# Kernel tuning notes

Measured on AMD Instinct MI355X. Metric: run time of the kernel, lower is better.

Reference implementation:

```python
import jax, jax.numpy as jnp
import numpy as np


def _conv2d(x, w, stride, padding):
    # x: NCHW, w: OIHW
    return jax.lax.conv_general_dilated(
        x, w, window_strides=(stride, stride),
        padding=((padding, padding), (padding, padding)),
        dimension_numbers=('NCHW', 'OIHW', 'NCHW'))


def setup_inputs() -> dict:
    key = jax.random.key(0)
    k1, k2 = jax.random.split(key)
    B, C_in, H, Wd = 8, 64, 256, 256
    C_out, ksz = 64, 3
    x = jax.random.normal(k1, (B, C_in, H, Wd), dtype=jnp.float32)
    W = jax.random.normal(k2, (C_out, C_in, ksz, ksz), dtype=jnp.float32)
    b = jnp.zeros((C_out,), dtype=jnp.float32)
    return {"x": x, "W": W, "b": b}


def reference(x, W, b):
    stride, padding = 1, 1
    B, C, H, Wd = x.shape
    # per-pixel (across-channel) normalization of activations
    xf = jnp.transpose(x, (0, 2, 3, 1)).reshape(-1, C)       # [B*H*W, C]
    mu = jnp.mean(xf, axis=-1, keepdims=True)
    var = jnp.mean((xf - mu) ** 2, axis=-1, keepdims=True)    # unbiased=False
    r = 1.0 / jnp.sqrt(var + 1e-8)
    y_norm = r * (xf - mu)
    # int8 fake-quant per pixel
    s_act = 127.0 / jnp.maximum(jnp.max(jnp.abs(y_norm), axis=-1, keepdims=True), 1e-8)
    y_tilde = jnp.clip(jnp.round(s_act * y_norm), -128.0, 127.0) / s_act
    y4 = jnp.transpose(y_tilde.reshape(B, H, Wd, C), (0, 3, 1, 2))
    # ternary weight quant (value; STE only matters for backward)
    s_w = 1.0 / jnp.maximum(jnp.mean(jnp.abs(W)), 1e-8)
    w_tilde = jnp.clip(jnp.round(s_w * W), -1.0, 1.0) / s_w
    out = _conv2d(y4, w_tilde, stride, padding) + b[None, :, None, None]
    return out
```

## Files before the change

kernel.cpp:

```cpp
#include <hip/hip_runtime.h>
#include <hip/hip_bf16.h>

typedef _Float16 half8 __attribute__((ext_vector_type(8)));
typedef float    f32x4 __attribute__((ext_vector_type(4)));

#define NB   8
#define NC   64
#define NH   256
#define NW   256
#define NO   64
#define Y_OFF    0ull
#define Y_BYTES  (33554432ull * 2ull)
#define TW_OFF   (Y_OFF + Y_BYTES)
#define TW_BYTES (576ull * 64ull * 2ull)
#define MSW_OFF  (TW_OFF + TW_BYTES)

__global__ __launch_bounds__(256) void wq_kernel(const float* __restrict__ W,
                                                 _Float16* __restrict__ tw2,
                                                 float* __restrict__ msw_out) {
    __shared__ float red[256];
    __shared__ float sw_sh;
    int tid = threadIdx.x;
    float s = 0.0f;
    #pragma unroll
    for (int i = 0; i < 144; ++i) s += fabsf(W[i * 256 + tid]);
    red[tid] = s;
    __syncthreads();
    for (int off = 128; off > 0; off >>= 1) {
        if (tid < off) red[tid] += red[tid + off];
        __syncthreads();
    }
    if (tid == 0) {
        float mean = red[0] / 36864.0f;
        float msw  = fmaxf(mean, 1e-8f);
        sw_sh      = 1.0f / msw;
        msw_out[0] = msw;
    }
    __syncthreads();
    float s_w = sw_sh;
    #pragma unroll
    for (int i = 0; i < 144; ++i) {
        int idx = i * 256 + tid;
        float t = rintf(s_w * W[idx]);
        t = fminf(1.0f, fmaxf(-1.0f, t));
        int o  = idx / 576;
        int r  = idx - o * 576;
        int c  = r / 9;
        int r2 = r - c * 9;
        int kh = r2 / 3;
        int kw = r2 - kh * 3;
        int k  = (kh * 3 + kw) * 64 + c;
        tw2[((k >> 3) * 64 + o) * 8 + (k & 7)] = (_Float16)t;
    }
}

__global__ __launch_bounds__(256, 2) void norm_kernel(const float* __restrict__ x,
                                                      _Float16* __restrict__ y) {
    int p  = blockIdx.x * 256 + threadIdx.x;
    int bb = p >> 16;
    int hw = p & 65535;
    const float* xp = x + (size_t)bb * 64 * 65536 + hw;

    float v[64];
    float s = 0.0f;
    #pragma unroll
    for (int c = 0; c < 64; ++c) { v[c] = xp[(size_t)c * 65536]; s += v[c]; }
    float mu = s * (1.0f / 64.0f);

    float var = 0.0f, dmax = 0.0f;
    #pragma unroll
    for (int c = 0; c < 64; ++c) {
        float d = v[c] - mu;
        var += d * d;
        dmax = fmaxf(dmax, fabsf(d));
    }
    var *= (1.0f / 64.0f);
    float r    = 1.0f / sqrtf(var + 1e-8f);
    float amax = fmaxf(dmax * r, 1e-8f);
    float s_a  = 127.0f / amax;
    float invs = amax / 127.0f;

    half8 hv[8];
    #pragma unroll
    for (int c = 0; c < 64; ++c) {
        float yn = (v[c] - mu) * r;
        float q  = rintf(s_a * yn);
        q = fminf(127.0f, fmaxf(-128.0f, q));
        hv[c >> 3][c & 7] = (_Float16)(q * invs);
    }
    half8* yp = (half8*)(y + (size_t)p * 64);
    #pragma unroll
    for (int j = 0; j < 8; ++j) yp[j] = hv[j];
}

__global__ __launch_bounds__(256, 2) void conv_kernel(const _Float16* __restrict__ y,
                                                      const _Float16* __restrict__ tw2,
                                                      const float* __restrict__ msw_p,
                                                      const float* __restrict__ bias,
                                                      float* __restrict__ out) {
    __shared__ alignas(16) _Float16 lds[3 * 8 * 66 * 8];

    int tid = threadIdx.x;
    int bid = blockIdx.x;
    int wt = bid & 3;
    int h  = (bid >> 2) & 255;
    int bb = bid >> 10;
    int w0 = wt * 64;

    for (int i = tid; i < 1584; i += 256) {
        int cc = i & 7;
        int t8 = i >> 3;
        int wl = t8 % 66;
        int kh = t8 / 66;
        int hp = h + kh - 1;
        int wp = w0 + wl - 1;
        half8 val;
        #pragma unroll
        for (int e = 0; e < 8; ++e) val[e] = (_Float16)0.0f;
        if ((unsigned)hp < 256u && (unsigned)wp < 256u)
            val = *(const half8*)(y + ((((size_t)bb * 256 + hp) * 256 + wp) * 64 + cc * 8));
        *(half8*)(lds + ((kh * 8 + cc) * 66 + wl) * 8) = val;
    }

    int l   = tid & 63;
    int wv  = tid >> 6;
    int l15 = l & 15;
    int q8  = l >> 4;

    half8 aw[18];
    #pragma unroll
    for (int ks = 0; ks < 18; ++ks)
        aw[ks] = *(const half8*)(tw2 + (((ks * 4 + q8) * 64) + wv * 16 + l15) * 8);

    __syncthreads();

    f32x4 acc[4];
    #pragma unroll
    for (int nt = 0; nt < 4; ++nt)
        #pragma unroll
        for (int r2 = 0; r2 < 4; ++r2) acc[nt][r2] = 0.0f;

    #pragma unroll
    for (int ks = 0; ks < 18; ++ks) {
        int tap = ks >> 1;
        int kh  = tap / 3;
        int kw  = tap - kh * 3;
        int ccb = (ks & 1) * 4 + q8;
        int base = ((kh * 8 + ccb) * 66 + kw + l15) * 8;
        #pragma unroll
        for (int nt = 0; nt < 4; ++nt) {
            half8 bf = *(const half8*)(lds + base + nt * 128);
            acc[nt] = __builtin_amdgcn_mfma_f32_16x16x32_f16(aw[ks], bf, acc[nt], 0, 0, 0);
        }
    }

    float msw = *msw_p;
    size_t obase = ((size_t)bb * 64) * 65536 + (size_t)h * 256;
    #pragma unroll
    for (int reg = 0; reg < 4; ++reg) {
        int o = wv * 16 + q8 * 4 + reg;
        float bo = bias[o];
        #pragma unroll
        for (int nt = 0; nt < 4; ++nt) {
            int w = w0 + nt * 16 + l15;
            out[obase + (size_t)o * 65536 + w] = acc[nt][reg] * msw + bo;
        }
    }
}

extern "C" void kernel_launch(void* const* d_in, const int* in_sizes, int n_in,
                              void* d_out, int out_size, void* d_ws, size_t ws_size,
                              hipStream_t stream) {
    const float* x = (const float*)d_in[0];
    const float* W = (const float*)d_in[1];
    const float* b = (const float*)d_in[2];
    float* out = (float*)d_out;

    char* ws = (char*)d_ws;
    _Float16* y   = (_Float16*)(ws + Y_OFF);
    _Float16* tw2 = (_Float16*)(ws + TW_OFF);
    float*    msw = (float*)(ws + MSW_OFF);

    wq_kernel<<<1, 256, 0, stream>>>(W, tw2, msw);
    norm_kernel<<<2048, 256, 0, stream>>>(x, y);
    conv_kernel<<<8192, 256, 0, stream>>>(y, tw2, msw, b, out);
}
```

Measured before the change: 315.9 us.

## Split weight quant, halve per-thread channels in norm, compute two output rows per conv block

Weight quantization is split into a vectorized reduction kernel plus a 144-block parallel write kernel, replacing the single-block serial scatter. The norm kernel now splits each pixel's 64 channels across two half-waves and combines the statistics with shuffles, which halves register pressure and doubles the grid. The conv kernel stages four input rows in a channel-padded LDS layout and computes two output rows per block, so halo rows are reused and total global loads of y drop. The cost is an extra launch and a larger LDS footprint per block, which may reduce occupancy.

```diff
diff --git a/kernel.cpp b/kernel.cpp
--- a/kernel.cpp
+++ b/kernel.cpp
@@ -4,122 +4,125 @@
 typedef _Float16 half8 __attribute__((ext_vector_type(8)));
 typedef float    f32x4 __attribute__((ext_vector_type(4)));
 
-#define NB   8
-#define NC   64
-#define NH   256
-#define NW   256
-#define NO   64
 #define Y_OFF    0ull
 #define Y_BYTES  (33554432ull * 2ull)
 #define TW_OFF   (Y_OFF + Y_BYTES)
 #define TW_BYTES (576ull * 64ull * 2ull)
 #define MSW_OFF  (TW_OFF + TW_BYTES)
 
-__global__ __launch_bounds__(256) void wq_kernel(const float* __restrict__ W,
-                                                 _Float16* __restrict__ tw2,
+__global__ __launch_bounds__(256) void wq_reduce(const float* __restrict__ W,
                                                  float* __restrict__ msw_out) {
     __shared__ float red[256];
-    __shared__ float sw_sh;
     int tid = threadIdx.x;
+    const float4* W4 = (const float4*)W;
     float s = 0.0f;
     #pragma unroll
-    for (int i = 0; i < 144; ++i) s += fabsf(W[i * 256 + tid]);
+    for (int i = 0; i < 36; ++i) {
+        float4 w = W4[i * 256 + tid];
+        s += fabsf(w.x) + fabsf(w.y) + fabsf(w.z) + fabsf(w.w);
+    }
     red[tid] = s;
     __syncthreads();
     for (int off = 128; off > 0; off >>= 1) {
         if (tid < off) red[tid] += red[tid + off];
         __syncthreads();
     }
-    if (tid == 0) {
-        float mean = red[0] / 36864.0f;
-        float msw  = fmaxf(mean, 1e-8f);
-        sw_sh      = 1.0f / msw;
-        msw_out[0] = msw;
-    }
-    __syncthreads();
-    float s_w = sw_sh;
-    #pragma unroll
-    for (int i = 0; i < 144; ++i) {
-        int idx = i * 256 + tid;
-        float t = rintf(s_w * W[idx]);
-        t = fminf(1.0f, fmaxf(-1.0f, t));
-        int o  = idx / 576;
-        int r  = idx - o * 576;
-        int c  = r / 9;
-        int r2 = r - c * 9;
-        int kh = r2 / 3;
-        int kw = r2 - kh * 3;
-        int k  = (kh * 3 + kw) * 64 + c;
-        tw2[((k >> 3) * 64 + o) * 8 + (k & 7)] = (_Float16)t;
-    }
+    if (tid == 0) msw_out[0] = fmaxf(red[0] / 36864.0f, 1e-8f);
 }
 
-__global__ __launch_bounds__(256, 2) void norm_kernel(const float* __restrict__ x,
-                                                      _Float16* __restrict__ y) {
-    int p  = blockIdx.x * 256 + threadIdx.x;
-    int bb = p >> 16;
-    int hw = p & 65535;
-    const float* xp = x + (size_t)bb * 64 * 65536 + hw;
+__global__ __launch_bounds__(256) void wq_write(const float* __restrict__ W,
+                                                const float* __restrict__ msw_p,
+                                                _Float16* __restrict__ tw2) {
+    int idx = blockIdx.x * 256 + threadIdx.x;
+    float s_w = 1.0f / msw_p[0];
+    float t = rintf(s_w * W[idx]);
+    t = fminf(1.0f, fmaxf(-1.0f, t));
+    int o  = idx / 576;
+    int r  = idx - o * 576;
+    int c  = r / 9;
+    int r2 = r - c * 9;
+    int kh = r2 / 3;
+    int kw = r2 - kh * 3;
+    int k  = (kh * 3 + kw) * 64 + c;
+    tw2[((k >> 3) * 64 + o) * 8 + (k & 7)] = (_Float16)t;
+}
 
-    float v[64];
+__global__ __launch_bounds__(256) void norm_kernel(const float* __restrict__ x,
+                                                   _Float16* __restrict__ y) {
+    int wave = threadIdx.x >> 6;
+    int l    = threadIdx.x & 63;
+    int pl   = l & 31;
+    int hh   = l >> 5;
+    int pg   = blockIdx.x * 4 + wave;
+    int p0   = pg * 32;
+    int bb   = p0 >> 16;
+    int hw   = (p0 & 65535) + pl;
+    const float* xp = x + ((size_t)bb * 64 + hh * 32) * 65536 + hw;
+
+    float v[32];
     float s = 0.0f;
     #pragma unroll
-    for (int c = 0; c < 64; ++c) { v[c] = xp[(size_t)c * 65536]; s += v[c]; }
+    for (int c = 0; c < 32; ++c) { v[c] = xp[(size_t)c * 65536]; s += v[c]; }
+    s += __shfl_xor(s, 32);
     float mu = s * (1.0f / 64.0f);
 
     float var = 0.0f, dmax = 0.0f;
     #pragma unroll
-    for (int c = 0; c < 64; ++c) {
+    for (int c = 0; c < 32; ++c) {
         float d = v[c] - mu;
         var += d * d;
         dmax = fmaxf(dmax, fabsf(d));
     }
-    var *= (1.0f / 64.0f);
+    var  += __shfl_xor(var, 32);
+    dmax  = fmaxf(dmax, __shfl_xor(dmax, 32));
+    var  *= (1.0f / 64.0f);
     float r    = 1.0f / sqrtf(var + 1e-8f);
     float amax = fmaxf(dmax * r, 1e-8f);
     float s_a  = 127.0f / amax;
     float invs = amax / 127.0f;
 
-    half8 hv[8];
+    half8 hv[4];
     #pragma unroll
-    for (int c = 0; c < 64; ++c) {
+    for (int c = 0; c < 32; ++c) {
         float yn = (v[c] - mu) * r;
         float q  = rintf(s_a * yn);
         q = fminf(127.0f, fmaxf(-128.0f, q));
         hv[c >> 3][c & 7] = (_Float16)(q * invs);
     }
-    half8* yp = (half8*)(y + (size_t)p * 64);
+    half8* yp = (half8*)(y + ((size_t)(p0 + pl) * 64) + hh * 32);
     #pragma unroll
-    for (int j = 0; j < 8; ++j) yp[j] = hv[j];
+    for (int j = 0; j < 4; ++j) yp[j] = hv[j];
 }
 
+#define CPAD 66
 __global__ __launch_bounds__(256, 2) void conv_kernel(const _Float16* __restrict__ y,
                                                       const _Float16* __restrict__ tw2,
                                                       const float* __restrict__ msw_p,
                                                       const float* __restrict__ bias,
                                                       float* __restrict__ out) {
-    __shared__ alignas(16) _Float16 lds[3 * 8 * 66 * 8];
+    __shared__ alignas(16) _Float16 lds[4 * 66 * CPAD];
 
     int tid = threadIdx.x;
     int bid = blockIdx.x;
     int wt = bid & 3;
-    int h  = (bid >> 2) & 255;
-    int bb = bid >> 10;
+    int hb = (bid >> 2) & 127;
+    int bb = bid >> 9;
     int w0 = wt * 64;
+    int h0 = hb * 2;
 
-    for (int i = tid; i < 1584; i += 256) {
+    for (int i = tid; i < 2112; i += 256) {
         int cc = i & 7;
         int t8 = i >> 3;
         int wl = t8 % 66;
-        int kh = t8 / 66;
-        int hp = h + kh - 1;
+        int r  = t8 / 66;
+        int hp = h0 + r - 1;
         int wp = w0 + wl - 1;
         half8 val;
         #pragma unroll
         for (int e = 0; e < 8; ++e) val[e] = (_Float16)0.0f;
         if ((unsigned)hp < 256u && (unsigned)wp < 256u)
             val = *(const half8*)(y + ((((size_t)bb * 256 + hp) * 256 + wp) * 64 + cc * 8));
-        *(half8*)(lds + ((kh * 8 + cc) * 66 + wl) * 8) = val;
+        *(half8*)(lds + (r * 66 + wl) * CPAD + cc * 8) = val;
     }
 
     int l   = tid & 63;
@@ -134,36 +137,40 @@
 
     __syncthreads();
 
-    f32x4 acc[4];
+    float msw = *msw_p;
     #pragma unroll
-    for (int nt = 0; nt < 4; ++nt)
+    for (int rr = 0; rr < 2; ++rr) {
+        f32x4 acc[4];
         #pragma unroll
-        for (int r2 = 0; r2 < 4; ++r2) acc[nt][r2] = 0.0f;
+        for (int nt = 0; nt < 4; ++nt)
+            #pragma unroll
+            for (int e = 0; e < 4; ++e) acc[nt][e] = 0.0f;
 
-    #pragma unroll
-    for (int ks = 0; ks < 18; ++ks) {
-        int tap = ks >> 1;
-        int kh  = tap / 3;
-        int kw  = tap - kh * 3;
-        int ccb = (ks & 1) * 4 + q8;
-        int base = ((kh * 8 + ccb) * 66 + kw + l15) * 8;
         #pragma unroll
-        for (int nt = 0; nt < 4; ++nt) {
-            half8 bf = *(const half8*)(lds + base + nt * 128);
-            acc[nt] = __builtin_amdgcn_mfma_f32_16x16x32_f16(aw[ks], bf, acc[nt], 0, 0, 0);
+        for (int ks = 0; ks < 18; ++ks) {
+            int tap = ks >> 1;
+            int kh  = tap / 3;
+            int kw  = tap - kh * 3;
+            int cbase = (ks & 1) * 32 + q8 * 8;
+            const _Float16* lrow = lds + ((rr + kh) * 66 + kw + l15) * CPAD + cbase;
+            #pragma unroll
+            for (int nt = 0; nt < 4; ++nt) {
+                half8 bf = *(const half8*)(lrow + nt * 16 * CPAD);
+                acc[nt] = __builtin_amdgcn_mfma_f32_16x16x32_f16(aw[ks], bf, acc[nt], 0, 0, 0);
+            }
         }
-    }
 
-    float msw = *msw_p;
-    size_t obase = ((size_t)bb * 64) * 65536 + (size_t)h * 256;
-    #pragma unroll
-    for (int reg = 0; reg < 4; ++reg) {
-        int o = wv * 16 + q8 * 4 + reg;
-        float bo = bias[o];
+        int hout = h0 + rr;
+        size_t obase = ((size_t)bb * 64) * 65536 + (size_t)hout * 256;
         #pragma unroll
-        for (int nt = 0; nt < 4; ++nt) {
-            int w = w0 + nt * 16 + l15;
-            out[obase + (size_t)o * 65536 + w] = acc[nt][reg] * msw + bo;
+        for (int reg = 0; reg < 4; ++reg) {
+            int o = wv * 16 + q8 * 4 + reg;
+            float bo = bias[o];
+            #pragma unroll
+            for (int nt = 0; nt < 4; ++nt) {
+                int w = w0 + nt * 16 + l15;
+                out[obase + (size_t)o * 65536 + w] = acc[nt][reg] * msw + bo;
+            }
         }
     }
 }
@@ -181,7 +188,8 @@
     _Float16* tw2 = (_Float16*)(ws + TW_OFF);
     float*    msw = (float*)(ws + MSW_OFF);
 
-    wq_kernel<<<1, 256, 0, stream>>>(W, tw2, msw);
-    norm_kernel<<<2048, 256, 0, stream>>>(x, y);
-    conv_kernel<<<8192, 256, 0, stream>>>(y, tw2, msw, b, out);
+    wq_reduce<<<1, 256, 0, stream>>>(W, msw);
+    wq_write<<<144, 256, 0, stream>>>(W, msw, tw2);
+    norm_kernel<<<4096, 256, 0, stream>>>(x, y);
+    conv_kernel<<<4096, 256, 0, stream>>>(y, tw2, msw, b, out);
 }
```

After: 500.5 us. +58.4%, slower.
